# Performance work log

Measured on AMD Instinct MI355X. Metric: run time of the kernel, lower is better.

Reference implementation:

```python
import jax, jax.numpy as jnp
import numpy as np

H0, H1, NHID, BATCH = 256, 256, 512, 2048

def setup_inputs() -> dict:
    key = jax.random.key(0)
    k1, k2, k3, k4, k5 = jax.random.split(key, 5)
    initrange = 0.1
    inputs = jax.random.normal(k1, (BATCH, NHID), dtype=jnp.float32)
    labels = jax.random.randint(k2, (BATCH,), 0, H1, dtype=jnp.int32)
    parent_labels = jax.random.randint(k3, (BATCH,), 0, H0, dtype=jnp.int32)
    layer_top_W = jax.random.uniform(k4, (NHID, H0), jnp.float32, -initrange, initrange)
    layer_top_b = jnp.zeros((H0,), jnp.float32)
    layer_bottom_W = jax.random.uniform(k5, (H0, NHID, H1), jnp.float32, -initrange, initrange)
    layer_bottom_b = jnp.zeros((H0, H1), jnp.float32)
    return {"inputs": inputs, "labels": labels, "parent_labels": parent_labels,
            "layer_top_W": layer_top_W, "layer_top_b": layer_top_b,
            "layer_bottom_W": layer_bottom_W, "layer_bottom_b": layer_bottom_b}

def reference(inputs, labels, parent_labels, layer_top_W, layer_top_b,
              layer_bottom_W, layer_bottom_b):
    batch = inputs.shape[0]
    # top-level softmax over coarse classes: [B, H0]
    top_probs = jax.nn.softmax(inputs @ layer_top_W + layer_top_b, axis=1)
    # per-sample gather of expert weight slice [B, NHID, H1] then bmm
    Wb = layer_bottom_W[parent_labels]            # [B, NHID, H1]
    bb = layer_bottom_b[parent_labels]            # [B, H1]
    bottom_logits = jnp.einsum('bd,bdk->bk', inputs, Wb) + bb
    bottom_probs = jax.nn.softmax(bottom_logits, axis=1)
    ar = jnp.arange(batch)
    target_probs = top_probs[ar, parent_labels] * bottom_probs[ar, labels]
    return target_probs
```

## Files before the change

### kernel.cpp

```cpp
#include <hip/hip_runtime.h>

constexpr int BATCH = 2048;
constexpr int NHID  = 512;
constexpr int H0    = 256;
constexpr int H1    = 256;
constexpr int S     = 8;
constexpr int J     = 3;

__global__ __launch_bounds__(128) void hs_8s(
    const float* __restrict__ x,
    const int*   __restrict__ labels,
    const int*   __restrict__ parents,
    const float* __restrict__ topW,
    const float* __restrict__ topb,
    const float* __restrict__ botW,
    const float* __restrict__ botb,
    float*       __restrict__ out)
{
    const int p = blockIdx.x / J;
    const int j = blockIdx.x % J;
    const int t = threadIdx.x;
    const int g = t >> 6;
    const int l = t & 63;

    __shared__ int   list[BATCH];
    __shared__ int   wcnt[2];
    __shared__ __align__(16) float xs[S][NHID];
    __shared__ float psm[2][S];

    int running = 0;
    for (int c = 0; c < BATCH; c += 128) {
        const bool match = (parents[c + t] == p);
        const unsigned long long mask = __ballot(match);
        if (l == 0) wcnt[g] = __popcll(mask);
        __syncthreads();
        const int off = running + (g ? wcnt[0] : 0);
        if (match)
            list[off + __popcll(mask & ((1ull << l) - 1ull))] = c + t;
        running += wcnt[0] + wcnt[1];
        __syncthreads();
    }
    const int n = running;
    if (n <= j * S) return;

    const float* Wbase = g ? botW + (size_t)p * NHID * H1 : topW;
    const float4 b4    = g ? *(const float4*)(botb + (size_t)p * H1 + 4 * l)
                           : *(const float4*)(topb + 4 * l);

    for (int base = j * S; base < n; base += J * S) {
        const int rem = min(S, n - base);

        for (int s = 0; s < S; ++s) {
            const int idx = list[base + min(s, rem - 1)];
            ((float4*)xs[s])[t] = ((const float4*)(x + (size_t)idx * NHID))[t];
        }

        int tgts[S];
        #pragma unroll
        for (int s = 0; s < S; ++s) {
            const int slot = base + min(s, rem - 1);
            tgts[s] = g ? labels[list[slot]] : p;
        }
        __syncthreads();

        float4 acc[S];
        #pragma unroll
        for (int s = 0; s < S; ++s) acc[s] = make_float4(0.f, 0.f, 0.f, 0.f);

        const float* Wp = Wbase + 4 * l;
        float4 ring[8];
        #pragma unroll
        for (int i = 0; i < 8; ++i)
            ring[i] = *(const float4*)(Wp + (size_t)i * H0);

        for (int d = 0; d < NHID; d += 8) {
            #pragma unroll
            for (int h = 0; h < 2; ++h) {
                const int dd = d + 4 * h;
                const float4 w0 = ring[4 * h + 0], w1 = ring[4 * h + 1];
                const float4 w2 = ring[4 * h + 2], w3 = ring[4 * h + 3];
                if (dd + 8 < NHID) {
                    #pragma unroll
                    for (int i = 0; i < 4; ++i)
                        ring[4 * h + i] =
                            *(const float4*)(Wp + (size_t)(dd + 8 + i) * H0);
                }
                #pragma unroll
                for (int s = 0; s < S; ++s) {
                    const float4 xv = *(const float4*)&xs[s][dd];
                    float4 a = acc[s];
                    a.x = fmaf(xv.x, w0.x, a.x); a.y = fmaf(xv.x, w0.y, a.y);
                    a.z = fmaf(xv.x, w0.z, a.z); a.w = fmaf(xv.x, w0.w, a.w);
                    a.x = fmaf(xv.y, w1.x, a.x); a.y = fmaf(xv.y, w1.y, a.y);
                    a.z = fmaf(xv.y, w1.z, a.z); a.w = fmaf(xv.y, w1.w, a.w);
                    a.x = fmaf(xv.z, w2.x, a.x); a.y = fmaf(xv.z, w2.y, a.y);
                    a.z = fmaf(xv.z, w2.z, a.z); a.w = fmaf(xv.z, w2.w, a.w);
                    a.x = fmaf(xv.w, w3.x, a.x); a.y = fmaf(xv.w, w3.y, a.y);
                    a.z = fmaf(xv.w, w3.z, a.z); a.w = fmaf(xv.w, w3.w, a.w);
                    acc[s] = a;
                }
            }
        }

        #pragma unroll
        for (int s = 0; s < S; ++s) {
            float4 v = acc[s];
            v.x += b4.x; v.y += b4.y; v.z += b4.z; v.w += b4.w;

            float m = fmaxf(fmaxf(v.x, v.y), fmaxf(v.z, v.w));
            #pragma unroll
            for (int off = 32; off > 0; off >>= 1)
                m = fmaxf(m, __shfl_xor(m, off, 64));

            const float ex = expf(v.x - m), ey = expf(v.y - m);
            const float ez = expf(v.z - m), ew = expf(v.w - m);
            float sum = (ex + ey) + (ez + ew);
            #pragma unroll
            for (int off = 32; off > 0; off >>= 1)
                sum += __shfl_xor(sum, off, 64);

            const int tgt = tgts[s];
            const int k   = tgt & 3;
            const float ev = (k == 0) ? ex : (k == 1) ? ey : (k == 2) ? ez : ew;
            if (l == (tgt >> 2))
                psm[g][s] = ev / sum;
        }
        __syncthreads();

        if (t < rem) {
            const int idx = list[base + t];
            out[idx] = psm[0][t] * psm[1][t];
        }
        __syncthreads();
    }
}

extern "C" void kernel_launch(void* const* d_in, const int* in_sizes, int n_in,
                              void* d_out, int out_size, void* d_ws, size_t ws_size,
                              hipStream_t stream) {
    const float* x       = (const float*)d_in[0];
    const int*   labels  = (const int*)  d_in[1];
    const int*   parents = (const int*)  d_in[2];
    const float* topW    = (const float*)d_in[3];
    const float* topb    = (const float*)d_in[4];
    const float* botW    = (const float*)d_in[5];
    const float* botb    = (const float*)d_in[6];
    float*       out     = (float*)d_out;

    hs_8s<<<H0 * J, 128, 0, stream>>>(x, labels, parents,
                                      topW, topb, botW, botb, out);
}
```

Measured before the change: 228.8 us.

## Split reduction dimension across warps and batch up to 32 samples per block

Replaces the three-blocks-per-parent scheme with one 512-thread block per parent. The NHID reduction is split four ways across waves, and up to 32 matching samples are processed per pass, so each weight slice is streamed once per 32 samples instead of once per 8. Partial sums are combined through shared memory before the softmax. The cost is a large shared footprint (xs 64KB plus reduction buffers), 128 accumulator registers per thread with occupancy pressure, and more block-wide barriers.

```diff
diff --git a/kernel.cpp b/kernel.cpp
--- a/kernel.cpp
+++ b/kernel.cpp
@@ -4,10 +4,10 @@
 constexpr int NHID  = 512;
 constexpr int H0    = 256;
 constexpr int H1    = 256;
-constexpr int S     = 8;
-constexpr int J     = 3;
+constexpr int SMAX  = 32;
+constexpr int KS    = NHID / 4;
 
-__global__ __launch_bounds__(128) void hs_8s(
+__global__ __launch_bounds__(512, 2) void hs_ksplit(
     const float* __restrict__ x,
     const int*   __restrict__ labels,
     const int*   __restrict__ parents,
@@ -17,115 +17,158 @@
     const float* __restrict__ botb,
     float*       __restrict__ out)
 {
-    const int p = blockIdx.x / J;
-    const int j = blockIdx.x % J;
-    const int t = threadIdx.x;
-    const int g = t >> 6;
-    const int l = t & 63;
+    const int p  = blockIdx.x;
+    const int t  = threadIdx.x;
+    const int g  = t >> 6;
+    const int l  = t & 63;
+    const int kw = g & 3;
+    const bool bot = (g < 4);
 
-    __shared__ int   list[BATCH];
-    __shared__ int   wcnt[2];
-    __shared__ __align__(16) float xs[S][NHID];
-    __shared__ float psm[2][S];
+    __shared__ int list[BATCH];
+    __shared__ int wcnt[8];
+    __shared__ __align__(16) float  xs[SMAX][NHID];
+    __shared__ __align__(16) float4 redB[3][4][64];
+    __shared__ __align__(16) float4 redT[3][4][64];
+    __shared__ float psm[2][SMAX];
 
     int running = 0;
-    for (int c = 0; c < BATCH; c += 128) {
+    for (int c = 0; c < BATCH; c += 512) {
         const bool match = (parents[c + t] == p);
         const unsigned long long mask = __ballot(match);
         if (l == 0) wcnt[g] = __popcll(mask);
         __syncthreads();
-        const int off = running + (g ? wcnt[0] : 0);
+        int off = running;
+        #pragma unroll
+        for (int w = 0; w < 8; ++w) {
+            const int cw = wcnt[w];
+            if (w < g) off += cw;
+            running += cw;
+        }
         if (match)
             list[off + __popcll(mask & ((1ull << l) - 1ull))] = c + t;
-        running += wcnt[0] + wcnt[1];
         __syncthreads();
     }
     const int n = running;
-    if (n <= j * S) return;
+    if (n == 0) return;
 
-    const float* Wbase = g ? botW + (size_t)p * NHID * H1 : topW;
-    const float4 b4    = g ? *(const float4*)(botb + (size_t)p * H1 + 4 * l)
-                           : *(const float4*)(topb + 4 * l);
+    const float* Wbase = bot
+        ? botW + (size_t)p * NHID * H1 + (size_t)kw * KS * H1
+        : topW + (size_t)kw * KS * H0;
+    const float4 b4 = bot ? *(const float4*)(botb + (size_t)p * H1 + 4 * l)
+                          : *(const float4*)(topb + 4 * l);
+    const int koff = kw * KS;
 
-    for (int base = j * S; base < n; base += J * S) {
-        const int rem = min(S, n - base);
+    for (int base = 0; base < n; base += SMAX) {
+        const int rem  = min(SMAX, n - base);
+        const int ngrp = (rem + 7) >> 3;
+        const int nrow = 8 * ngrp;
 
-        for (int s = 0; s < S; ++s) {
-            const int idx = list[base + min(s, rem - 1)];
-            ((float4*)xs[s])[t] = ((const float4*)(x + (size_t)idx * NHID))[t];
-        }
-
-        int tgts[S];
-        #pragma unroll
-        for (int s = 0; s < S; ++s) {
-            const int slot = base + min(s, rem - 1);
-            tgts[s] = g ? labels[list[slot]] : p;
+        for (int s0 = 0; s0 < nrow; s0 += 4) {
+            const int row = s0 + (t >> 7);
+            const int idx = list[base + min(row, rem - 1)];
+            ((float4*)xs[row])[t & 127] =
+                ((const float4*)(x + (size_t)idx * NHID))[t & 127];
         }
         __syncthreads();
 
-        float4 acc[S];
+        float4 acc[4][8];
         #pragma unroll
-        for (int s = 0; s < S; ++s) acc[s] = make_float4(0.f, 0.f, 0.f, 0.f);
+        for (int gr = 0; gr < 4; ++gr)
+            #pragma unroll
+            for (int s = 0; s < 8; ++s)
+                acc[gr][s] = make_float4(0.f, 0.f, 0.f, 0.f);
 
         const float* Wp = Wbase + 4 * l;
         float4 ring[8];
         #pragma unroll
         for (int i = 0; i < 8; ++i)
-            ring[i] = *(const float4*)(Wp + (size_t)i * H0);
+            ring[i] = *(const float4*)(Wp + (size_t)i * 256);
 
-        for (int d = 0; d < NHID; d += 8) {
+        for (int d = 0; d < KS; d += 8) {
             #pragma unroll
             for (int h = 0; h < 2; ++h) {
                 const int dd = d + 4 * h;
                 const float4 w0 = ring[4 * h + 0], w1 = ring[4 * h + 1];
                 const float4 w2 = ring[4 * h + 2], w3 = ring[4 * h + 3];
-                if (dd + 8 < NHID) {
+                if (dd + 8 < KS) {
                     #pragma unroll
                     for (int i = 0; i < 4; ++i)
                         ring[4 * h + i] =
-                            *(const float4*)(Wp + (size_t)(dd + 8 + i) * H0);
+                            *(const float4*)(Wp + (size_t)(dd + 8 + i) * 256);
                 }
                 #pragma unroll
-                for (int s = 0; s < S; ++s) {
-                    const float4 xv = *(const float4*)&xs[s][dd];
-                    float4 a = acc[s];
-                    a.x = fmaf(xv.x, w0.x, a.x); a.y = fmaf(xv.x, w0.y, a.y);
-                    a.z = fmaf(xv.x, w0.z, a.z); a.w = fmaf(xv.x, w0.w, a.w);
-                    a.x = fmaf(xv.y, w1.x, a.x); a.y = fmaf(xv.y, w1.y, a.y);
-                    a.z = fmaf(xv.y, w1.z, a.z); a.w = fmaf(xv.y, w1.w, a.w);
-                    a.x = fmaf(xv.z, w2.x, a.x); a.y = fmaf(xv.z, w2.y, a.y);
-                    a.z = fmaf(xv.z, w2.z, a.z); a.w = fmaf(xv.z, w2.w, a.w);
-                    a.x = fmaf(xv.w, w3.x, a.x); a.y = fmaf(xv.w, w3.y, a.y);
-                    a.z = fmaf(xv.w, w3.z, a.z); a.w = fmaf(xv.w, w3.w, a.w);
-                    acc[s] = a;
+                for (int gr = 0; gr < 4; ++gr) {
+                    if (gr < ngrp) {
+                        #pragma unroll
+                        for (int s = 0; s < 8; ++s) {
+                            const float4 xv =
+                                *(const float4*)&xs[8 * gr + s][koff + dd];
+                            float4 a = acc[gr][s];
+                            a.x = fmaf(xv.x, w0.x, a.x); a.y = fmaf(xv.x, w0.y, a.y);
+                            a.z = fmaf(xv.x, w0.z, a.z); a.w = fmaf(xv.x, w0.w, a.w);
+                            a.x = fmaf(xv.y, w1.x, a.x); a.y = fmaf(xv.y, w1.y, a.y);
+                            a.z = fmaf(xv.y, w1.z, a.z); a.w = fmaf(xv.y, w1.w, a.w);
+                            a.x = fmaf(xv.z, w2.x, a.x); a.y = fmaf(xv.z, w2.y, a.y);
+                            a.z = fmaf(xv.z, w2.z, a.z); a.w = fmaf(xv.z, w2.w, a.w);
+                            a.x = fmaf(xv.w, w3.x, a.x); a.y = fmaf(xv.w, w3.y, a.y);
+                            a.z = fmaf(xv.w, w3.z, a.z); a.w = fmaf(xv.w, w3.w, a.w);
+                            acc[gr][s] = a;
+                        }
+                    }
                 }
             }
         }
 
+        float4 (*red)[4][64] = bot ? redB : redT;
         #pragma unroll
-        for (int s = 0; s < S; ++s) {
-            float4 v = acc[s];
-            v.x += b4.x; v.y += b4.y; v.z += b4.z; v.w += b4.w;
+        for (int gr = 0; gr < 4; ++gr) {
+            if (gr < ngrp) {
+                #pragma unroll
+                for (int hf = 0; hf < 2; ++hf) {
+                    if (kw != 0) {
+                        #pragma unroll
+                        for (int si = 0; si < 4; ++si)
+                            red[kw - 1][si][l] = acc[gr][4 * hf + si];
+                    }
+                    __syncthreads();
+                    if (kw == 0) {
+                        #pragma unroll
+                        for (int si = 0; si < 4; ++si) {
+                            const int s = 8 * gr + 4 * hf + si;
+                            const float4 r0 = red[0][si][l];
+                            const float4 r1 = red[1][si][l];
+                            const float4 r2 = red[2][si][l];
+                            float4 v = acc[gr][4 * hf + si];
+                            v.x += r0.x + r1.x + r2.x + b4.x;
+                            v.y += r0.y + r1.y + r2.y + b4.y;
+                            v.z += r0.z + r1.z + r2.z + b4.z;
+                            v.w += r0.w + r1.w + r2.w + b4.w;
 
-            float m = fmaxf(fmaxf(v.x, v.y), fmaxf(v.z, v.w));
-            #pragma unroll
-            for (int off = 32; off > 0; off >>= 1)
-                m = fmaxf(m, __shfl_xor(m, off, 64));
+                            float m = fmaxf(fmaxf(v.x, v.y), fmaxf(v.z, v.w));
+                            #pragma unroll
+                            for (int off = 32; off > 0; off >>= 1)
+                                m = fmaxf(m, __shfl_xor(m, off, 64));
 
-            const float ex = expf(v.x - m), ey = expf(v.y - m);
-            const float ez = expf(v.z - m), ew = expf(v.w - m);
-            float sum = (ex + ey) + (ez + ew);
-            #pragma unroll
-            for (int off = 32; off > 0; off >>= 1)
-                sum += __shfl_xor(sum, off, 64);
+                            const float ex = expf(v.x - m), ey = expf(v.y - m);
+                            const float ez = expf(v.z - m), ew = expf(v.w - m);
+                            float sum = (ex + ey) + (ez + ew);
+                            #pragma unroll
+                            for (int off = 32; off > 0; off >>= 1)
+                                sum += __shfl_xor(sum, off, 64);
 
-            const int tgt = tgts[s];
-            const int k   = tgt & 3;
-            const float ev = (k == 0) ? ex : (k == 1) ? ey : (k == 2) ? ez : ew;
-            if (l == (tgt >> 2))
-                psm[g][s] = ev / sum;
+                            const int tgt =
+                                bot ? labels[list[base + min(s, rem - 1)]] : p;
+                            const int k = tgt & 3;
+                            const float ev = (k == 0) ? ex : (k == 1) ? ey
+                                           : (k == 2) ? ez : ew;
+                            if (l == (tgt >> 2))
+                                psm[bot ? 1 : 0][s] = ev / sum;
+                        }
+                    }
+                    __syncthreads();
+                }
+            }
         }
-        __syncthreads();
 
         if (t < rem) {
             const int idx = list[base + t];
@@ -147,6 +190,6 @@
     const float* botb    = (const float*)d_in[6];
     float*       out     = (float*)d_out;
 
-    hs_8s<<<H0 * J, 128, 0, stream>>>(x, labels, parents,
+    hs_ksplit<<<H0, 512, 0, stream>>>(x, labels, parents,
                                       topW, topb, botW, botb, out);
 }
```

Measured after the change: 228.7 us. About the same (-0.1%).

## Split the hidden-dim reduction across four waves per matrix with shared-memory combine

Applied to the files above, without the earlier changes.

Blocks grow from 128 to 512 threads, and each of the two GEMV roles (top and bottom) is split into four K-slices of 128 hidden units, each handled by its own wave. Partial accumulators go to shared memory, and wave 0 of each role reduces them and runs the softmax. The aim is to raise parallelism per block and shorten each wave's serial dependency chain over NHID, since the grid has only 768 blocks. The cost is more LDS use, an extra barrier, and the softmax now running on only a quarter of the waves.

```diff
diff --git a/kernel.cpp b/kernel.cpp
--- a/kernel.cpp
+++ b/kernel.cpp
@@ -6,8 +6,9 @@
 constexpr int H1    = 256;
 constexpr int S     = 8;
 constexpr int J     = 3;
+constexpr int KSL   = 128;
 
-__global__ __launch_bounds__(128) void hs_8s(
+__global__ __launch_bounds__(512) void hs_v6(
     const float* __restrict__ x,
     const int*   __restrict__ labels,
     const int*   __restrict__ parents,
@@ -17,49 +18,58 @@
     const float* __restrict__ botb,
     float*       __restrict__ out)
 {
-    const int p = blockIdx.x / J;
-    const int j = blockIdx.x % J;
-    const int t = threadIdx.x;
-    const int g = t >> 6;
-    const int l = t & 63;
+    const int p  = blockIdx.x / J;
+    const int j  = blockIdx.x % J;
+    const int t  = threadIdx.x;
+    const int g  = t >> 6;
+    const int l  = t & 63;
+    const int kq = g & 3;
+    const bool bot = (g < 4);
+    const int pi = bot ? 0 : 1;
+    const int po = bot ? 1 : 0;
 
-    __shared__ int   list[BATCH];
-    __shared__ int   wcnt[2];
-    __shared__ __align__(16) float xs[S][NHID];
+    __shared__ int list[BATCH];
+    __shared__ int wcnt[8];
+    __shared__ __align__(16) float  xs[S][NHID];
+    __shared__ __align__(16) float4 red[2][3][S][64];
     __shared__ float psm[2][S];
 
     int running = 0;
-    for (int c = 0; c < BATCH; c += 128) {
+    for (int c = 0; c < BATCH; c += 512) {
         const bool match = (parents[c + t] == p);
         const unsigned long long mask = __ballot(match);
         if (l == 0) wcnt[g] = __popcll(mask);
         __syncthreads();
-        const int off = running + (g ? wcnt[0] : 0);
+        int off = running;
+        #pragma unroll
+        for (int w = 0; w < 8; ++w) {
+            const int cw = wcnt[w];
+            if (w < g) off += cw;
+            running += cw;
+        }
         if (match)
             list[off + __popcll(mask & ((1ull << l) - 1ull))] = c + t;
-        running += wcnt[0] + wcnt[1];
         __syncthreads();
     }
     const int n = running;
     if (n <= j * S) return;
 
-    const float* Wbase = g ? botW + (size_t)p * NHID * H1 : topW;
-    const float4 b4    = g ? *(const float4*)(botb + (size_t)p * H1 + 4 * l)
-                           : *(const float4*)(topb + 4 * l);
+    const float* Wbase = bot
+        ? botW + (size_t)p * NHID * H1 + (size_t)kq * KSL * H1
+        : topW + (size_t)kq * KSL * H0;
+    const float4 b4 = bot ? *(const float4*)(botb + (size_t)p * H1 + 4 * l)
+                          : *(const float4*)(topb + 4 * l);
+    const int xoff = kq * KSL;
 
     for (int base = j * S; base < n; base += J * S) {
         const int rem = min(S, n - base);
 
-        for (int s = 0; s < S; ++s) {
-            const int idx = list[base + min(s, rem - 1)];
-            ((float4*)xs[s])[t] = ((const float4*)(x + (size_t)idx * NHID))[t];
-        }
-
-        int tgts[S];
         #pragma unroll
-        for (int s = 0; s < S; ++s) {
-            const int slot = base + min(s, rem - 1);
-            tgts[s] = g ? labels[list[slot]] : p;
+        for (int s0 = 0; s0 < S; s0 += 4) {
+            const int row = s0 + (t >> 7);
+            const int idx = list[base + min(row, rem - 1)];
+            ((float4*)xs[row])[t & 127] =
+                ((const float4*)(x + (size_t)idx * NHID))[t & 127];
         }
         __syncthreads();
 
@@ -71,23 +81,23 @@
         float4 ring[8];
         #pragma unroll
         for (int i = 0; i < 8; ++i)
-            ring[i] = *(const float4*)(Wp + (size_t)i * H0);
+            ring[i] = *(const float4*)(Wp + (size_t)i * 256);
 
-        for (int d = 0; d < NHID; d += 8) {
+        for (int d = 0; d < KSL; d += 8) {
             #pragma unroll
             for (int h = 0; h < 2; ++h) {
                 const int dd = d + 4 * h;
                 const float4 w0 = ring[4 * h + 0], w1 = ring[4 * h + 1];
                 const float4 w2 = ring[4 * h + 2], w3 = ring[4 * h + 3];
-                if (dd + 8 < NHID) {
+                if (dd + 8 < KSL) {
                     #pragma unroll
                     for (int i = 0; i < 4; ++i)
                         ring[4 * h + i] =
-                            *(const float4*)(Wp + (size_t)(dd + 8 + i) * H0);
+                            *(const float4*)(Wp + (size_t)(dd + 8 + i) * 256);
                 }
                 #pragma unroll
                 for (int s = 0; s < S; ++s) {
-                    const float4 xv = *(const float4*)&xs[s][dd];
+                    const float4 xv = *(const float4*)&xs[s][xoff + dd];
                     float4 a = acc[s];
                     a.x = fmaf(xv.x, w0.x, a.x); a.y = fmaf(xv.x, w0.y, a.y);
                     a.z = fmaf(xv.x, w0.z, a.z); a.w = fmaf(xv.x, w0.w, a.w);
@@ -102,28 +112,42 @@
             }
         }
 
-        #pragma unroll
-        for (int s = 0; s < S; ++s) {
-            float4 v = acc[s];
-            v.x += b4.x; v.y += b4.y; v.z += b4.z; v.w += b4.w;
+        if (kq != 0) {
+            #pragma unroll
+            for (int s = 0; s < S; ++s) red[pi][kq - 1][s][l] = acc[s];
+        }
+        __syncthreads();
+        if (kq == 0) {
+            #pragma unroll
+            for (int s = 0; s < S; ++s) {
+                const float4 r0 = red[pi][0][s][l];
+                const float4 r1 = red[pi][1][s][l];
+                const float4 r2 = red[pi][2][s][l];
+                float4 v = acc[s];
+                v.x += r0.x + r1.x + r2.x + b4.x;
+                v.y += r0.y + r1.y + r2.y + b4.y;
+                v.z += r0.z + r1.z + r2.z + b4.z;
+                v.w += r0.w + r1.w + r2.w + b4.w;
 
-            float m = fmaxf(fmaxf(v.x, v.y), fmaxf(v.z, v.w));
-            #pragma unroll
-            for (int off = 32; off > 0; off >>= 1)
-                m = fmaxf(m, __shfl_xor(m, off, 64));
+                float m = fmaxf(fmaxf(v.x, v.y), fmaxf(v.z, v.w));
+                #pragma unroll
+                for (int off = 32; off > 0; off >>= 1)
+                    m = fmaxf(m, __shfl_xor(m, off, 64));
 
-            const float ex = expf(v.x - m), ey = expf(v.y - m);
-            const float ez = expf(v.z - m), ew = expf(v.w - m);
-            float sum = (ex + ey) + (ez + ew);
-            #pragma unroll
-            for (int off = 32; off > 0; off >>= 1)
-                sum += __shfl_xor(sum, off, 64);
+                const float ex = expf(v.x - m), ey = expf(v.y - m);
+                const float ez = expf(v.z - m), ew = expf(v.w - m);
+                float sum = (ex + ey) + (ez + ew);
+                #pragma unroll
+                for (int off = 32; off > 0; off >>= 1)
+                    sum += __shfl_xor(sum, off, 64);
 
-            const int tgt = tgts[s];
-            const int k   = tgt & 3;
-            const float ev = (k == 0) ? ex : (k == 1) ? ey : (k == 2) ? ez : ew;
-            if (l == (tgt >> 2))
-                psm[g][s] = ev / sum;
+                const int tgt = bot ? labels[list[base + min(s, rem - 1)]] : p;
+                const int k   = tgt & 3;
+                const float ev = (k == 0) ? ex : (k == 1) ? ey
+                               : (k == 2) ? ez : ew;
+                if (l == (tgt >> 2))
+                    psm[po][s] = ev / sum;
+            }
         }
         __syncthreads();
 
@@ -147,6 +171,6 @@
     const float* botb    = (const float*)d_in[6];
     float*       out     = (float*)d_out;
 
-    hs_8s<<<H0 * J, 128, 0, stream>>>(x, labels, parents,
+    hs_v6<<<H0 * J, 512, 0, stream>>>(x, labels, parents,
                                       topW, topb, botW, botb, out);
 }
```

New measurement: 230.6 us. No clear change (+0.8%).
